# Optimization experiments

Measured on AMD Instinct MI355X. Metric: run time of the kernel, lower is better.

The kernel has to match this reference:

```python
import jax, jax.numpy as jnp
import numpy as np

N_HARMONIC = 6
CONCAT = (3,)  # cfg.append_distance: concat embedding after this layer index
N_LAYERS = 8


def harmonic_embedding(x):
    # x: [N, 3] -> [N, 6*2*3 + 3] = [N, 39]
    freqs = 2.0 ** jnp.arange(N_HARMONIC, dtype=x.dtype)  # omega0 = 1.0, logspace
    embed = (x[..., None] * freqs).reshape(*x.shape[:-1], -1)  # [N, 18]
    return jnp.concatenate([jnp.sin(embed), jnp.cos(embed), x], axis=-1)


def setup_inputs() -> dict:
    key = jax.random.key(0)
    N, H, E = 262144, 256, 39
    ks = jax.random.split(key, 11)
    inp = {"points": jax.random.normal(ks[0], (N, 3), dtype=jnp.float32)}
    in_dims = [E, H, H, H, E + H, H, H, H]  # skip-concat before layer 4
    for i, d_in in enumerate(in_dims):
        scale = 1.0 / np.sqrt(d_in)
        inp[f"w{i}"] = jax.random.normal(ks[i + 1], (d_in, H), dtype=jnp.float32) * scale
        inp[f"b{i}"] = jnp.zeros((H,), dtype=jnp.float32)
    inp["wsdf"] = jax.random.normal(ks[9], (H, 1), dtype=jnp.float32) * (1.0 / np.sqrt(H))
    inp["bsdf"] = jnp.zeros((1,), dtype=jnp.float32)
    return inp


def reference(points, w0, b0, w1, b1, w2, b2, w3, b3, w4, b4, w5, b5, w6, b6, w7, b7, wsdf, bsdf):
    ws = [w0, w1, w2, w3, w4, w5, w6, w7]
    bs = [b0, b1, b2, b3, b4, b5, b6, b7]
    emb = harmonic_embedding(points.reshape(-1, 3))  # [N, 39]
    x = emb
    for i in range(N_LAYERS):
        x = jax.nn.relu(x @ ws[i] + bs[i])
        if i in CONCAT:
            x = jnp.concatenate([emb, x], axis=-1)  # torch.cat([add, xyz])
    return x @ wsdf + bsdf  # [N, 1] signed distance
```

## Files before the change

### kernel.cpp

```cpp
#include <hip/hip_runtime.h>
#include <hip/hip_fp16.h>

typedef _Float16 f16x8 __attribute__((ext_vector_type(8)));
typedef _Float16 f16x4 __attribute__((ext_vector_type(4)));
typedef float    f32x16 __attribute__((ext_vector_type(16)));
typedef float    f32x4 __attribute__((ext_vector_type(4)));

#define SH 264
#define SE 56
#define PTS 64

struct LayerPtrs {
  const float* w[8];
  const float* b[8];
};

__global__ void prep_weights(LayerPtrs P, f16x8* __restrict__ wf) {
  int gid = blockIdx.x * 256 + threadIdx.x;
  if (gid >= 60416) return;
  const int OFF[9] = {0,1536,9728,17920,26112,35840,44032,52224,60416};
  int l = 0;
  while (gid >= OFF[l+1]) ++l;
  int f = gid - OFF[l];
  int lane = f & 63;
  int t = f >> 6;
  int mtile = t & 7;
  int kc = t >> 3;
  int col = mtile * 32 + (lane & 31);
  int kb  = (lane >> 5) * 8;
  const float* w = P.w[l];
  f16x8 v;
#pragma unroll
  for (int j = 0; j < 8; ++j) {
    float x = 0.f;
    if (l == 4) {
      if (kc < 3) {
        int k = kc * 16 + kb + j;
        if (k < 39) x = w[k * 256 + col];
      } else {
        int k = (kc - 3) * 16 + kb + j;
        x = w[(39 + k) * 256 + col];
      }
    } else if (l == 0) {
      int k = kc * 16 + kb + j;
      if (k < 39) x = w[k * 256 + col];
    } else {
      int k = kc * 16 + kb + j;
      x = w[k * 256 + col];
    }
    v[j] = (_Float16)x;
  }
  wf[gid] = v;
}

template<int NKC>
__device__ __forceinline__ void mm(const f16x8* __restrict__ wb,
                                   const _Float16* __restrict__ b0,
                                   const _Float16* __restrict__ b1,
                                   f32x16 acc[2][2]) {
#pragma unroll
  for (int kc = 0; kc < NKC; ++kc) {
    f16x8 a0 = wb[(kc * 8 + 0) * 64];
    f16x8 a1 = wb[(kc * 8 + 1) * 64];
    f16x8 v0 = *(const f16x8*)(b0 + kc * 16);
    f16x8 v1 = *(const f16x8*)(b1 + kc * 16);
    acc[0][0] = __builtin_amdgcn_mfma_f32_32x32x16_f16(a0, v0, acc[0][0], 0, 0, 0);
    acc[0][1] = __builtin_amdgcn_mfma_f32_32x32x16_f16(a0, v1, acc[0][1], 0, 0, 0);
    acc[1][0] = __builtin_amdgcn_mfma_f32_32x32x16_f16(a1, v0, acc[1][0], 0, 0, 0);
    acc[1][1] = __builtin_amdgcn_mfma_f32_32x32x16_f16(a1, v1, acc[1][1], 0, 0, 0);
  }
}

__device__ __forceinline__ void init_acc(f32x16 acc[2][2], const float* __restrict__ bp,
                                         int h) {
#pragma unroll
  for (int mt = 0; mt < 2; ++mt)
#pragma unroll
    for (int g = 0; g < 4; ++g) {
      f32x4 bv = *(const f32x4*)&bp[mt * 32 + 8 * g + 4 * h];
#pragma unroll
      for (int nt = 0; nt < 2; ++nt)
#pragma unroll
        for (int r = 0; r < 4; ++r)
          acc[mt][nt][4 * g + r] = bv[r];
    }
}

__device__ __forceinline__ void store_act(f32x16 acc[2][2], int wg,
                                          int lane, _Float16* __restrict__ H) {
  int p0 = lane & 31, h = lane >> 5;
#pragma unroll
  for (int mt = 0; mt < 2; ++mt) {
    int hb = wg * 64 + mt * 32 + 4 * h;
#pragma unroll
    for (int g = 0; g < 4; ++g) {
#pragma unroll
      for (int nt = 0; nt < 2; ++nt) {
        f16x4 o;
#pragma unroll
        for (int r = 0; r < 4; ++r)
          o[r] = (_Float16)fmaxf(acc[mt][nt][4 * g + r], 0.f);
        *(f16x4*)&H[(nt * 32 + p0) * SH + hb + 8 * g] = o;
      }
    }
  }
}

__global__ __launch_bounds__(256, 3)
void mlp_fused(const float* __restrict__ points,
               LayerPtrs P,
               const f16x8* __restrict__ wf,
               const float* __restrict__ wsdf,
               const float* __restrict__ bsdf,
               float* __restrict__ out) {
  __shared__ __align__(16) _Float16 H[PTS * SH];
  __shared__ __align__(16) _Float16 E[PTS * SE];
  const int tid = threadIdx.x;
  const int blk = blockIdx.x;

  if (tid < PTS) {
    int p = blk * PTS + tid;
    float xyz[3] = {points[p * 3 + 0], points[p * 3 + 1], points[p * 3 + 2]};
    _Float16* row = &E[tid * SE];
#pragma unroll
    for (int c = 0; c < 3; ++c) {
      float fr = 1.f;
#pragma unroll
      for (int k = 0; k < 6; ++k) {
        float e = xyz[c] * fr;
        row[c * 6 + k]      = (_Float16)sinf(e);
        row[18 + c * 6 + k] = (_Float16)cosf(e);
        fr *= 2.f;
      }
      row[36 + c] = (_Float16)xyz[c];
    }
#pragma unroll
    for (int c = 39; c < SE; ++c) row[c] = (_Float16)0.f;
  }
  __syncthreads();

  const int lane = tid & 63;
  const int wg   = tid >> 6;
  const int p0   = lane & 31;
  const int h    = lane >> 5;

  const _Float16* e0 = &E[p0 * SE + h * 8];
  const _Float16* e1 = &E[(32 + p0) * SE + h * 8];
  const _Float16* h0 = &H[p0 * SH + h * 8];
  const _Float16* h1 = &H[(32 + p0) * SH + h * 8];
  const f16x8* wb = wf + (wg * 2) * 64 + lane;

  const int WOFF[8] = {0,1536,9728,17920,26112,35840,44032,52224};

  f32x16 acc[2][2];

  init_acc(acc, P.b[0] + wg * 64, h);
  mm<3>(wb + WOFF[0], e0, e1, acc);
  store_act(acc, wg, lane, H);
  __syncthreads();

#pragma unroll
  for (int l = 1; l < 4; ++l) {
    init_acc(acc, P.b[l] + wg * 64, h);
    mm<16>(wb + WOFF[l], h0, h1, acc);
    __syncthreads();
    store_act(acc, wg, lane, H);
    __syncthreads();
  }

  init_acc(acc, P.b[4] + wg * 64, h);
  mm<3>(wb + WOFF[4], e0, e1, acc);
  mm<16>(wb + WOFF[4] + 3 * 512, h0, h1, acc);
  __syncthreads();
  store_act(acc, wg, lane, H);
  __syncthreads();

#pragma unroll
  for (int l = 5; l < 8; ++l) {
    init_acc(acc, P.b[l] + wg * 64, h);
    mm<16>(wb + WOFF[l], h0, h1, acc);
    __syncthreads();
    store_act(acc, wg, lane, H);
    __syncthreads();
  }

  {
    const int p = tid >> 2, part = tid & 3;
    float a = 0.f;
    const _Float16* xr = &H[p * SH + part * 64];
#pragma unroll
    for (int j = 0; j < 8; ++j) {
      f16x8 hh = *(const f16x8*)&xr[j * 8];
      f32x4 wa = *(const f32x4*)&wsdf[part * 64 + j * 8];
      f32x4 wc = *(const f32x4*)&wsdf[part * 64 + j * 8 + 4];
      a += (float)hh[0] * wa[0] + (float)hh[1] * wa[1]
         + (float)hh[2] * wa[2] + (float)hh[3] * wa[3]
         + (float)hh[4] * wc[0] + (float)hh[5] * wc[1]
         + (float)hh[6] * wc[2] + (float)hh[7] * wc[3];
    }
    a += __shfl_down(a, 1);
    a += __shfl_down(a, 2);
    if (part == 0) out[blk * PTS + p] = a + bsdf[0];
  }
}

extern "C" void kernel_launch(void* const* d_in, const int* in_sizes, int n_in,
                              void* d_out, int out_size, void* d_ws, size_t ws_size,
                              hipStream_t stream) {
  const float* points = (const float*)d_in[0];
  LayerPtrs P;
  for (int i = 0; i < 8; ++i) {
    P.w[i] = (const float*)d_in[1 + 2 * i];
    P.b[i] = (const float*)d_in[2 + 2 * i];
  }
  const float* wsdf = (const float*)d_in[17];
  const float* bsdf = (const float*)d_in[18];
  f16x8* wf = (f16x8*)d_ws;

  int N = in_sizes[0] / 3;
  prep_weights<<<236, 256, 0, stream>>>(P, wf);
  mlp_fused<<<N / PTS, 256, 0, stream>>>(points, P, wf, wsdf, bsdf, (float*)d_out);
}
```

Before: 356.3 us.

## Double points per block and give each wave a 128x64 output tile

After: 360.4 us. No clear change (+1.2%).

```diff
diff --git a/kernel.cpp b/kernel.cpp
--- a/kernel.cpp
+++ b/kernel.cpp
@@ -8,7 +8,7 @@
 
 #define SH 264
 #define SE 56
-#define PTS 64
+#define PTS 128
 
 struct LayerPtrs {
   const float* w[8];
@@ -57,24 +57,30 @@
 __device__ __forceinline__ void mm(const f16x8* __restrict__ wb,
                                    const _Float16* __restrict__ b0,
                                    const _Float16* __restrict__ b1,
-                                   f32x16 acc[2][2]) {
+                                   f32x16 acc[4][2]) {
 #pragma unroll
   for (int kc = 0; kc < NKC; ++kc) {
     f16x8 a0 = wb[(kc * 8 + 0) * 64];
     f16x8 a1 = wb[(kc * 8 + 1) * 64];
+    f16x8 a2 = wb[(kc * 8 + 2) * 64];
+    f16x8 a3 = wb[(kc * 8 + 3) * 64];
     f16x8 v0 = *(const f16x8*)(b0 + kc * 16);
     f16x8 v1 = *(const f16x8*)(b1 + kc * 16);
     acc[0][0] = __builtin_amdgcn_mfma_f32_32x32x16_f16(a0, v0, acc[0][0], 0, 0, 0);
     acc[0][1] = __builtin_amdgcn_mfma_f32_32x32x16_f16(a0, v1, acc[0][1], 0, 0, 0);
     acc[1][0] = __builtin_amdgcn_mfma_f32_32x32x16_f16(a1, v0, acc[1][0], 0, 0, 0);
     acc[1][1] = __builtin_amdgcn_mfma_f32_32x32x16_f16(a1, v1, acc[1][1], 0, 0, 0);
-  }
-}
-
-__device__ __forceinline__ void init_acc(f32x16 acc[2][2], const float* __restrict__ bp,
+    acc[2][0] = __builtin_amdgcn_mfma_f32_32x32x16_f16(a2, v0, acc[2][0], 0, 0, 0);
+    acc[2][1] = __builtin_amdgcn_mfma_f32_32x32x16_f16(a2, v1, acc[2][1], 0, 0, 0);
+    acc[3][0] = __builtin_amdgcn_mfma_f32_32x32x16_f16(a3, v0, acc[3][0], 0, 0, 0);
+    acc[3][1] = __builtin_amdgcn_mfma_f32_32x32x16_f16(a3, v1, acc[3][1], 0, 0, 0);
+  }
+}
+
+__device__ __forceinline__ void init_acc(f32x16 acc[4][2], const float* __restrict__ bp,
                                          int h) {
 #pragma unroll
-  for (int mt = 0; mt < 2; ++mt)
+  for (int mt = 0; mt < 4; ++mt)
 #pragma unroll
     for (int g = 0; g < 4; ++g) {
       f32x4 bv = *(const f32x4*)&bp[mt * 32 + 8 * g + 4 * h];
@@ -86,12 +92,12 @@
     }
 }
 
-__device__ __forceinline__ void store_act(f32x16 acc[2][2], int wg,
+__device__ __forceinline__ void store_act(f32x16 acc[4][2], int wg, int pg,
                                           int lane, _Float16* __restrict__ H) {
   int p0 = lane & 31, h = lane >> 5;
 #pragma unroll
-  for (int mt = 0; mt < 2; ++mt) {
-    int hb = wg * 64 + mt * 32 + 4 * h;
+  for (int mt = 0; mt < 4; ++mt) {
+    int hb = wg * 128 + mt * 32 + 4 * h;
 #pragma unroll
     for (int g = 0; g < 4; ++g) {
 #pragma unroll
@@ -100,13 +106,13 @@
 #pragma unroll
         for (int r = 0; r < 4; ++r)
           o[r] = (_Float16)fmaxf(acc[mt][nt][4 * g + r], 0.f);
-        *(f16x4*)&H[(nt * 32 + p0) * SH + hb + 8 * g] = o;
+        *(f16x4*)&H[(pg * 64 + nt * 32 + p0) * SH + hb + 8 * g] = o;
       }
     }
   }
 }
 
-__global__ __launch_bounds__(256, 3)
+__global__ __launch_bounds__(256, 2)
 void mlp_fused(const float* __restrict__ points,
                LayerPtrs P,
                const f16x8* __restrict__ wf,
@@ -140,66 +146,67 @@
   __syncthreads();
 
   const int lane = tid & 63;
-  const int wg   = tid >> 6;
+  const int wv   = tid >> 6;
+  const int wg   = wv & 1;
+  const int pg   = wv >> 1;
   const int p0   = lane & 31;
   const int h    = lane >> 5;
 
-  const _Float16* e0 = &E[p0 * SE + h * 8];
-  const _Float16* e1 = &E[(32 + p0) * SE + h * 8];
-  const _Float16* h0 = &H[p0 * SH + h * 8];
-  const _Float16* h1 = &H[(32 + p0) * SH + h * 8];
-  const f16x8* wb = wf + (wg * 2) * 64 + lane;
+  const _Float16* e0 = &E[(pg * 64 +  0 + p0) * SE + h * 8];
+  const _Float16* e1 = &E[(pg * 64 + 32 + p0) * SE + h * 8];
+  const _Float16* h0 = &H[(pg * 64 +  0 + p0) * SH + h * 8];
+  const _Float16* h1 = &H[(pg * 64 + 32 + p0) * SH + h * 8];
+  const f16x8* wb = wf + (wg * 4) * 64 + lane;
 
   const int WOFF[8] = {0,1536,9728,17920,26112,35840,44032,52224};
 
-  f32x16 acc[2][2];
-
-  init_acc(acc, P.b[0] + wg * 64, h);
+  f32x16 acc[4][2];
+
+  init_acc(acc, P.b[0] + wg * 128, h);
   mm<3>(wb + WOFF[0], e0, e1, acc);
-  store_act(acc, wg, lane, H);
+  store_act(acc, wg, pg, lane, H);
   __syncthreads();
 
 #pragma unroll
   for (int l = 1; l < 4; ++l) {
-    init_acc(acc, P.b[l] + wg * 64, h);
+    init_acc(acc, P.b[l] + wg * 128, h);
     mm<16>(wb + WOFF[l], h0, h1, acc);
     __syncthreads();
-    store_act(acc, wg, lane, H);
-    __syncthreads();
-  }
-
-  init_acc(acc, P.b[4] + wg * 64, h);
+    store_act(acc, wg, pg, lane, H);
+    __syncthreads();
+  }
+
+  init_acc(acc, P.b[4] + wg * 128, h);
   mm<3>(wb + WOFF[4], e0, e1, acc);
   mm<16>(wb + WOFF[4] + 3 * 512, h0, h1, acc);
   __syncthreads();
-  store_act(acc, wg, lane, H);
+  store_act(acc, wg, pg, lane, H);
   __syncthreads();
 
 #pragma unroll
   for (int l = 5; l < 8; ++l) {
-    init_acc(acc, P.b[l] + wg * 64, h);
+    init_acc(acc, P.b[l] + wg * 128, h);
     mm<16>(wb + WOFF[l], h0, h1, acc);
     __syncthreads();
-    store_act(acc, wg, lane, H);
+    store_act(acc, wg, pg, lane, H);
     __syncthreads();
   }
 
   {
-    const int p = tid >> 2, part = tid & 3;
+    const int p = tid >> 1, part = tid & 1;
     float a = 0.f;
-    const _Float16* xr = &H[p * SH + part * 64];
-#pragma unroll
-    for (int j = 0; j < 8; ++j) {
+    const _Float16* xr = &H[p * SH + part * 128];
+#pragma unroll
+    for (int j = 0; j < 16; ++j) {
       f16x8 hh = *(const f16x8*)&xr[j * 8];
-      f32x4 wa = *(const f32x4*)&wsdf[part * 64 + j * 8];
-      f32x4 wc = *(const f32x4*)&wsdf[part * 64 + j * 8 + 4];
+      f32x4 wa = *(const f32x4*)&wsdf[part * 128 + j * 8];
+      f32x4 wc = *(const f32x4*)&wsdf[part * 128 + j * 8 + 4];
       a += (float)hh[0] * wa[0] + (float)hh[1] * wa[1]
          + (float)hh[2] * wa[2] + (float)hh[3] * wa[3]
          + (float)hh[4] * wc[0] + (float)hh[5] * wc[1]
          + (float)hh[6] * wc[2] + (float)hh[7] * wc[3];
     }
     a += __shfl_down(a, 1);
-    a += __shfl_down(a, 2);
     if (part == 0) out[blk * PTS + p] = a + bsdf[0];
   }
 }
```

## Double points per block and switch LDS activations to k-chunk-major layout

Applied to the files above, without the earlier changes.

Result: faster. 317.9 us (-10.8%).

```diff
diff --git a/kernel.cpp b/kernel.cpp
--- a/kernel.cpp
+++ b/kernel.cpp
@@ -6,9 +6,7 @@
 typedef float    f32x16 __attribute__((ext_vector_type(16)));
 typedef float    f32x4 __attribute__((ext_vector_type(4)));
 
-#define SH 264
-#define SE 56
-#define PTS 64
+#define PTS 128
 
 struct LayerPtrs {
   const float* w[8];
@@ -55,23 +53,28 @@
 
 template<int NKC>
 __device__ __forceinline__ void mm(const f16x8* __restrict__ wb,
-                                   const _Float16* __restrict__ b0,
-                                   const _Float16* __restrict__ b1,
-                                   f32x16 acc[2][2]) {
+                                   const f16x8* __restrict__ b,
+                                   f32x16 acc[2][4]) {
 #pragma unroll
   for (int kc = 0; kc < NKC; ++kc) {
     f16x8 a0 = wb[(kc * 8 + 0) * 64];
     f16x8 a1 = wb[(kc * 8 + 1) * 64];
-    f16x8 v0 = *(const f16x8*)(b0 + kc * 16);
-    f16x8 v1 = *(const f16x8*)(b1 + kc * 16);
+    f16x8 v0 = b[kc * 2 * PTS + 0];
+    f16x8 v1 = b[kc * 2 * PTS + 32];
+    f16x8 v2 = b[kc * 2 * PTS + 64];
+    f16x8 v3 = b[kc * 2 * PTS + 96];
     acc[0][0] = __builtin_amdgcn_mfma_f32_32x32x16_f16(a0, v0, acc[0][0], 0, 0, 0);
     acc[0][1] = __builtin_amdgcn_mfma_f32_32x32x16_f16(a0, v1, acc[0][1], 0, 0, 0);
+    acc[0][2] = __builtin_amdgcn_mfma_f32_32x32x16_f16(a0, v2, acc[0][2], 0, 0, 0);
+    acc[0][3] = __builtin_amdgcn_mfma_f32_32x32x16_f16(a0, v3, acc[0][3], 0, 0, 0);
     acc[1][0] = __builtin_amdgcn_mfma_f32_32x32x16_f16(a1, v0, acc[1][0], 0, 0, 0);
     acc[1][1] = __builtin_amdgcn_mfma_f32_32x32x16_f16(a1, v1, acc[1][1], 0, 0, 0);
-  }
-}
-
-__device__ __forceinline__ void init_acc(f32x16 acc[2][2], const float* __restrict__ bp,
+    acc[1][2] = __builtin_amdgcn_mfma_f32_32x32x16_f16(a1, v2, acc[1][2], 0, 0, 0);
+    acc[1][3] = __builtin_amdgcn_mfma_f32_32x32x16_f16(a1, v3, acc[1][3], 0, 0, 0);
+  }
+}
+
+__device__ __forceinline__ void init_acc(f32x16 acc[2][4], const float* __restrict__ bp,
                                          int h) {
 #pragma unroll
   for (int mt = 0; mt < 2; ++mt)
@@ -79,49 +82,49 @@
     for (int g = 0; g < 4; ++g) {
       f32x4 bv = *(const f32x4*)&bp[mt * 32 + 8 * g + 4 * h];
 #pragma unroll
-      for (int nt = 0; nt < 2; ++nt)
+      for (int nt = 0; nt < 4; ++nt)
 #pragma unroll
         for (int r = 0; r < 4; ++r)
           acc[mt][nt][4 * g + r] = bv[r];
     }
 }
 
-__device__ __forceinline__ void store_act(f32x16 acc[2][2], int wg,
-                                          int lane, _Float16* __restrict__ H) {
+__device__ __forceinline__ void store_act(f32x16 acc[2][4], int wv,
+                                          int lane, f16x8* __restrict__ HB) {
   int p0 = lane & 31, h = lane >> 5;
 #pragma unroll
   for (int mt = 0; mt < 2; ++mt) {
-    int hb = wg * 64 + mt * 32 + 4 * h;
 #pragma unroll
     for (int g = 0; g < 4; ++g) {
-#pragma unroll
-      for (int nt = 0; nt < 2; ++nt) {
+      int c = wv * 8 + mt * 4 + g;
+#pragma unroll
+      for (int nt = 0; nt < 4; ++nt) {
         f16x4 o;
 #pragma unroll
         for (int r = 0; r < 4; ++r)
           o[r] = (_Float16)fmaxf(acc[mt][nt][4 * g + r], 0.f);
-        *(f16x4*)&H[(nt * 32 + p0) * SH + hb + 8 * g] = o;
+        *(f16x4*)((_Float16*)&HB[c * PTS + nt * 32 + p0] + 4 * h) = o;
       }
     }
   }
 }
 
-__global__ __launch_bounds__(256, 3)
+__global__ __launch_bounds__(256, 2)
 void mlp_fused(const float* __restrict__ points,
                LayerPtrs P,
                const f16x8* __restrict__ wf,
                const float* __restrict__ wsdf,
                const float* __restrict__ bsdf,
                float* __restrict__ out) {
-  __shared__ __align__(16) _Float16 H[PTS * SH];
-  __shared__ __align__(16) _Float16 E[PTS * SE];
+  __shared__ __align__(16) f16x8 HB[32 * PTS];
+  __shared__ __align__(16) f16x8 EB[6 * PTS];
   const int tid = threadIdx.x;
   const int blk = blockIdx.x;
 
   if (tid < PTS) {
     int p = blk * PTS + tid;
     float xyz[3] = {points[p * 3 + 0], points[p * 3 + 1], points[p * 3 + 2]};
-    _Float16* row = &E[tid * SE];
+    _Float16 row[48];
 #pragma unroll
     for (int c = 0; c < 3; ++c) {
       float fr = 1.f;
@@ -135,71 +138,70 @@
       row[36 + c] = (_Float16)xyz[c];
     }
 #pragma unroll
-    for (int c = 39; c < SE; ++c) row[c] = (_Float16)0.f;
+    for (int c = 39; c < 48; ++c) row[c] = (_Float16)0.f;
+#pragma unroll
+    for (int c = 0; c < 6; ++c)
+      EB[c * PTS + tid] = *(const f16x8*)&row[c * 8];
   }
   __syncthreads();
 
   const int lane = tid & 63;
-  const int wg   = tid >> 6;
+  const int wv   = tid >> 6;
   const int p0   = lane & 31;
   const int h    = lane >> 5;
 
-  const _Float16* e0 = &E[p0 * SE + h * 8];
-  const _Float16* e1 = &E[(32 + p0) * SE + h * 8];
-  const _Float16* h0 = &H[p0 * SH + h * 8];
-  const _Float16* h1 = &H[(32 + p0) * SH + h * 8];
-  const f16x8* wb = wf + (wg * 2) * 64 + lane;
+  const f16x8* eb = &EB[h * PTS + p0];
+  const f16x8* hb = &HB[h * PTS + p0];
+  const f16x8* wb = wf + (wv * 2) * 64 + lane;
 
   const int WOFF[8] = {0,1536,9728,17920,26112,35840,44032,52224};
 
-  f32x16 acc[2][2];
-
-  init_acc(acc, P.b[0] + wg * 64, h);
-  mm<3>(wb + WOFF[0], e0, e1, acc);
-  store_act(acc, wg, lane, H);
+  f32x16 acc[2][4];
+
+  init_acc(acc, P.b[0] + wv * 64, h);
+  mm<3>(wb + WOFF[0], eb, acc);
+  store_act(acc, wv, lane, HB);
   __syncthreads();
 
 #pragma unroll
   for (int l = 1; l < 4; ++l) {
-    init_acc(acc, P.b[l] + wg * 64, h);
-    mm<16>(wb + WOFF[l], h0, h1, acc);
-    __syncthreads();
-    store_act(acc, wg, lane, H);
-    __syncthreads();
-  }
-
-  init_acc(acc, P.b[4] + wg * 64, h);
-  mm<3>(wb + WOFF[4], e0, e1, acc);
-  mm<16>(wb + WOFF[4] + 3 * 512, h0, h1, acc);
-  __syncthreads();
-  store_act(acc, wg, lane, H);
+    init_acc(acc, P.b[l] + wv * 64, h);
+    mm<16>(wb + WOFF[l], hb, acc);
+    __syncthreads();
+    store_act(acc, wv, lane, HB);
+    __syncthreads();
+  }
+
+  init_acc(acc, P.b[4] + wv * 64, h);
+  mm<3>(wb + WOFF[4], eb, acc);
+  mm<16>(wb + WOFF[4] + 3 * 512, hb, acc);
+  __syncthreads();
+  store_act(acc, wv, lane, HB);
   __syncthreads();
 
 #pragma unroll
   for (int l = 5; l < 8; ++l) {
-    init_acc(acc, P.b[l] + wg * 64, h);
-    mm<16>(wb + WOFF[l], h0, h1, acc);
-    __syncthreads();
-    store_act(acc, wg, lane, H);
+    init_acc(acc, P.b[l] + wv * 64, h);
+    mm<16>(wb + WOFF[l], hb, acc);
+    __syncthreads();
+    store_act(acc, wv, lane, HB);
     __syncthreads();
   }
 
   {
-    const int p = tid >> 2, part = tid & 3;
+    const int p = tid >> 1, part = tid & 1;
     float a = 0.f;
-    const _Float16* xr = &H[p * SH + part * 64];
-#pragma unroll
-    for (int j = 0; j < 8; ++j) {
-      f16x8 hh = *(const f16x8*)&xr[j * 8];
-      f32x4 wa = *(const f32x4*)&wsdf[part * 64 + j * 8];
-      f32x4 wc = *(const f32x4*)&wsdf[part * 64 + j * 8 + 4];
+#pragma unroll
+    for (int c2 = 0; c2 < 16; ++c2) {
+      f16x8 hh = HB[(part * 16 + c2) * PTS + p];
+      f32x4 wa = *(const f32x4*)&wsdf[(part * 16 + c2) * 8];
+      f32x4 wc = *(const f32x4*)&wsdf[(part * 16 + c2) * 8 + 4];
       a += (float)hh[0] * wa[0] + (float)hh[1] * wa[1]
          + (float)hh[2] * wa[2] + (float)hh[3] * wa[3]
          + (float)hh[4] * wc[0] + (float)hh[5] * wc[1]
          + (float)hh[6] * wc[2] + (float)hh[7] * wc[3];
     }
     a += __shfl_down(a, 1);
-    a += __shfl_down(a, 2);
     if (part == 0) out[blk * PTS + p] = a + bsdf[0];
   }
 }
```
